# Optimization experiments

Hardware: AMD Instinct MI355X
Metric: run time of the kernel (lower is better)

## Reference

```python
import jax, jax.numpy as jnp
import numpy as np

N_NODES = 50000
N_EDGES = 1_600_000
IN_DIM, OUT_DIM, N_HEADS = 256, 64, 4
EPS = 1e-12  # F.normalize eps


def setup_inputs() -> dict:
    key = jax.random.key(0)
    k1, k2, k3, k4, k5 = jax.random.split(key, 5)
    h = jax.random.normal(k1, (N_NODES, IN_DIM), dtype=jnp.float32)
    edge_index = jax.random.randint(k2, (2, N_EDGES), 0, N_NODES, dtype=jnp.int32)
    # small scale keeps exp(leaky_relu(.)) well-conditioned (mimics xavier init)
    W = jax.random.normal(k3, (IN_DIM, OUT_DIM), dtype=jnp.float32) * 0.05
    Wl = jax.random.normal(k4, (N_HEADS, OUT_DIM), dtype=jnp.float32) * 0.05
    Wr = jax.random.normal(k5, (N_HEADS, OUT_DIM), dtype=jnp.float32) * 0.05
    b = jnp.zeros((OUT_DIM,), dtype=jnp.float32)
    return {"h": h, "W": W, "Wl": Wl, "Wr": Wr, "b": b, "edge_index": edge_index}


def reference(h, W, Wl, Wr, b, edge_index):
    N = h.shape[0]
    H = Wl.shape[0]
    x = h @ W                      # [N, D]
    el = x @ Wl.T                  # [N, H]
    er = x @ Wr.T                  # [N, H]
    src, dst = edge_index[0], edge_index[1]
    e = el[src] + er[dst]          # [E, H]
    e = jnp.exp(jax.nn.leaky_relu(e, negative_slope=0.2))
    # L1 row normalization over edges == F.normalize(dense_scatter, p=1, dim=-1)
    rowsum = jax.ops.segment_sum(e, src, num_segments=N)          # [N, H]
    w = e / jnp.maximum(rowsum, EPS)[src]                          # [E, H]
    # SpMM aggregation, per head to bound peak memory
    heads = [jax.ops.segment_sum(w[:, hd:hd + 1] * x[dst], src, num_segments=N)
             for hd in range(H)]
    out = jnp.stack(heads, axis=1)                                 # [N, H, D]
    out = jax.nn.elu(out + b)
    return out.reshape(N, H * x.shape[1])                          # [N, H*D]
```

## Files before the change

kernel.cpp:

```cpp
#include <hip/hip_runtime.h>
#include <hip/hip_bf16.h>
#include <hip/hip_fp16.h>

#define N_NODES 50000
#define N_EDGES 1600000
#define NPB    50
#define NBUK   1000
#define NSL    8
#define BCAPS  320
#define BCAPH  1280
#define GEMMB  782
#define PARTB  512
#define CHUNK  3125
#define BD     8

typedef __attribute__((ext_vector_type(8))) short short8;
typedef __attribute__((ext_vector_type(4))) float f32x4;

__device__ __forceinline__ unsigned short f2bf(float f) {
  union { float f; unsigned int i; } v; v.f = f;
  unsigned int i = v.i;
  unsigned int r = i + 0x7FFFu + ((i >> 16) & 1u);
  return (unsigned short)(r >> 16);
}

__global__ __launch_bounds__(256) void k_xpart(const float* __restrict__ hmat,
    const float* __restrict__ Wmat,
    const float* __restrict__ Wl, const float* __restrict__ Wr,
    float* __restrict__ el, float* __restrict__ er,
    __half* __restrict__ x16,
    const int* __restrict__ ei, int* __restrict__ bcnt,
    unsigned int* __restrict__ raw) {
  __shared__ __align__(16) char smem[36864];
  const int t = threadIdx.x;
  if (blockIdx.x >= PARTB) {
    unsigned short* Wt = (unsigned short*)smem;
    for (int idx = t; idx < 64 * 256; idx += 256) {
      int k = idx >> 6, n = idx & 63;
      Wt[n * 264 + k] = f2bf(Wmat[idx]);
    }
    __syncthreads();
    const int wave = t >> 6, lane = t & 63;
    const int quad = lane >> 4, l16 = lane & 15;
    const int m0 = (blockIdx.x - PARTB) * 64 + wave * 16;
    int arow = m0 + l16; if (arow >= N_NODES) arow = N_NODES - 1;
    f32x4 c[4] = {{0,0,0,0},{0,0,0,0},{0,0,0,0},{0,0,0,0}};
    const float* aptr = hmat + (size_t)arow * 256 + quad * 8;
    #pragma unroll
    for (int kb = 0; kb < 8; ++kb) {
      f32x4 a0 = *(const f32x4*)(aptr + kb * 32);
      f32x4 a1 = *(const f32x4*)(aptr + kb * 32 + 4);
      short8 a;
      a[0] = (short)f2bf(a0[0]); a[1] = (short)f2bf(a0[1]);
      a[2] = (short)f2bf(a0[2]); a[3] = (short)f2bf(a0[3]);
      a[4] = (short)f2bf(a1[0]); a[5] = (short)f2bf(a1[1]);
      a[6] = (short)f2bf(a1[2]); a[7] = (short)f2bf(a1[3]);
      #pragma unroll
      for (int nt = 0; nt < 4; ++nt) {
        int n = nt * 16 + l16;
        short8 b = *(const short8*)(&Wt[n * 264 + kb * 32 + quad * 8]);
        c[nt] = __builtin_amdgcn_mfma_f32_16x16x32_bf16(a, b, c[nt], 0, 0, 0);
      }
    }
    float wlv[4][4], wrv[4][4];
    #pragma unroll
    for (int h = 0; h < 4; ++h)
      #pragma unroll
      for (int nt = 0; nt < 4; ++nt) {
        wlv[h][nt] = Wl[h * 64 + nt * 16 + l16];
        wrv[h][nt] = Wr[h * 64 + nt * 16 + l16];
      }
    #pragma unroll
    for (int r = 0; r < 4; ++r) {
      const int grow = m0 + quad * 4 + r;
      const bool ok = grow < N_NODES;
      #pragma unroll
      for (int nt = 0; nt < 4; ++nt)
        if (ok) x16[grow * 64 + nt * 16 + l16] = __float2half(c[nt][r]);
      #pragma unroll
      for (int h = 0; h < 4; ++h) {
        float pl = c[0][r] * wlv[h][0];
        pl = fmaf(c[1][r], wlv[h][1], pl);
        pl = fmaf(c[2][r], wlv[h][2], pl);
        pl = fmaf(c[3][r], wlv[h][3], pl);
        float pr = c[0][r] * wrv[h][0];
        pr = fmaf(c[1][r], wrv[h][1], pr);
        pr = fmaf(c[2][r], wrv[h][2], pr);
        pr = fmaf(c[3][r], wrv[h][3], pr);
        #pragma unroll
        for (int off = 1; off < 16; off <<= 1) {
          pl += __shfl_xor(pl, off, 64);
          pr += __shfl_xor(pr, off, 64);
        }
        if (ok && l16 == 0) { el[grow * 4 + h] = pl; er[grow * 4 + h] = pr; }
      }
    }
  } else {
    int* scnt = (int*)smem;
    unsigned int* sbin = (unsigned int*)(smem + 4000);
    const int pj = blockIdx.x;
    const int slice = blockIdx.x & 7;
    for (int i = t; i < NBUK; i += 256) scnt[i] = 0;
    __syncthreads();
    const int e0 = pj * CHUNK;
    for (int e = e0 + t; e < e0 + CHUNK; e += 256) {
      int s = ei[e], d = ei[N_EDGES + e];
      int b = s / NPB;
      int sl = s - b * NPB;
      unsigned int val = ((unsigned int)d << 8) | (unsigned int)sl;
      int p = atomicAdd(&scnt[b], 1);
      if (p < BD) {
        sbin[b * BD + p] = val;
      } else {
        int cell = b * NSL + slice;
        int gp = atomicAdd(&bcnt[cell * 16], 1);
        if (gp < BCAPS) raw[(size_t)cell * BCAPS + gp] = val;
      }
    }
    __syncthreads();
    for (int b = t; b < NBUK; b += 256) {
      int c = scnt[b]; if (c > BD) c = BD;
      if (c > 0) {
        int cell = b * NSL + slice;
        int gp = atomicAdd(&bcnt[cell * 16], c);
        for (int k = 0; k < c; ++k) {
          int idx = gp + k;
          if (idx < BCAPS) raw[(size_t)cell * BCAPS + idx] = sbin[b * BD + k];
        }
      }
    }
  }
}

__global__ __launch_bounds__(256) void k_bucket(const unsigned int* __restrict__ raw,
    const int* __restrict__ bcnt,
    const float* __restrict__ el, const float* __restrict__ er,
    int* __restrict__ dlist, uint2* __restrict__ wts,
    int* __restrict__ rs_s, int* __restrict__ rs_e) {
  __shared__ unsigned int sraw[BCAPH];
  __shared__ int pref[NPB + 1];
  __shared__ int cur[NPB];
  const int b = blockIdx.x >> 1, H = blockIdx.x & 1, t = threadIdx.x;
  const int s0 = H * 4;
  int c0 = bcnt[(b * NSL + s0 + 0) * 16]; if (c0 > BCAPS) c0 = BCAPS;
  int c1 = bcnt[(b * NSL + s0 + 1) * 16]; if (c1 > BCAPS) c1 = BCAPS;
  int c2 = bcnt[(b * NSL + s0 + 2) * 16]; if (c2 > BCAPS) c2 = BCAPS;
  int c3 = bcnt[(b * NSL + s0 + 3) * 16]; if (c3 > BCAPS) c3 = BCAPS;
  const int o1 = c0, o2 = c0 + c1, o3 = c0 + c1 + c2, cnt = o3 + c3;
  if (t <= NPB) pref[t] = 0;
  __syncthreads();
  for (int j = t; j < c0; j += 256) { unsigned int r = raw[(size_t)(b*NSL+s0+0)*BCAPS + j]; sraw[j]      = r; atomicAdd(&pref[(int)(r & 255u) + 1], 1); }
  for (int j = t; j < c1; j += 256) { unsigned int r = raw[(size_t)(b*NSL+s0+1)*BCAPS + j]; sraw[o1 + j] = r; atomicAdd(&pref[(int)(r & 255u) + 1], 1); }
  for (int j = t; j < c2; j += 256) { unsigned int r = raw[(size_t)(b*NSL+s0+2)*BCAPS + j]; sraw[o2 + j] = r; atomicAdd(&pref[(int)(r & 255u) + 1], 1); }
  for (int j = t; j < c3; j += 256) { unsigned int r = raw[(size_t)(b*NSL+s0+3)*BCAPS + j]; sraw[o3 + j] = r; atomicAdd(&pref[(int)(r & 255u) + 1], 1); }
  __syncthreads();
  if (t == 0) {
    int run = 0;
    #pragma unroll
    for (int n = 0; n <= NPB; ++n) { run += pref[n]; pref[n] = run; }
  }
  __syncthreads();
  const int wbase = (b * 2 + H) * BCAPH;
  if (t < NPB) {
    cur[t] = pref[t];
    rs_s[H * N_NODES + b * NPB + t] = wbase + pref[t];
    rs_e[H * N_NODES + b * NPB + t] = wbase + pref[t + 1];
  }
  __syncthreads();
  const int base = b * NPB;
  for (int j = t; j < cnt; j += 256) {
    unsigned int r = sraw[j];
    int sl = (int)(r & 255u);
    int d  = (int)(r >> 8);
    int pos = atomicAdd(&cur[sl], 1);
    f32x4 a = ((const f32x4*)el)[base + sl];
    f32x4 e = ((const f32x4*)er)[d];
    float w[4];
    #pragma unroll
    for (int hh = 0; hh < 4; ++hh) {
      float tt = a[hh] + e[hh];
      tt = (tt >= 0.f) ? tt : 0.2f * tt;
      w[hh] = __expf(tt);
    }
    union { __half2 h; unsigned int i; } u01, u23;
    u01.h = __floats2half2_rn(w[0], w[1]);
    u23.h = __floats2half2_rn(w[2], w[3]);
    dlist[wbase + pos] = d;
    wts[wbase + pos] = make_uint2(u01.i, u23.i);
  }
}

__global__ __launch_bounds__(256) void k_agg(const __half* __restrict__ x16,
    const int* __restrict__ rs_s, const int* __restrict__ rs_e,
    const int* __restrict__ dlist, const uint2* __restrict__ wts,
    const float* __restrict__ bvec, float* __restrict__ out) {
  const int node = (blockIdx.x * 256 + threadIdx.x) >> 6;
  const int lane = threadIdx.x & 63;
  if (node >= N_NODES) return;
  float n0 = 0.f, n1 = 0.f, n2 = 0.f, n3 = 0.f;
  float d0 = 0.f, d1 = 0.f, d2 = 0.f, d3 = 0.f;
  #pragma unroll
  for (int hf = 0; hf < 2; ++hf) {
    const int j0 = __builtin_amdgcn_readfirstlane(rs_s[hf * N_NODES + node]);
    const int j1 = __builtin_amdgcn_readfirstlane(rs_e[hf * N_NODES + node]);
    #pragma unroll 4
    for (int j = j0; j < j1; ++j) {
      const int dd = dlist[j];
      const uint2 hw = wts[j];
      union { unsigned int i; __half2 h; } u01, u23;
      u01.i = hw.x; u23.i = hw.y;
      float2 f01 = __half22float2(u01.h);
      float2 f23 = __half22float2(u23.h);
      const __half* rowp = x16 + ((size_t)dd << 6);
      float xv = __half2float(rowp[lane]);
      d0 += f01.x; d1 += f01.y; d2 += f23.x; d3 += f23.y;
      n0 = fmaf(f01.x, xv, n0); n1 = fmaf(f01.y, xv, n1);
      n2 = fmaf(f23.x, xv, n2); n3 = fmaf(f23.y, xv, n3);
    }
  }
  float bv = bvec[lane];
  size_t ob = (size_t)node * 256 + lane;
  float o;
  o = n0 / fmaxf(d0, 1e-12f) + bv; o = (o > 0.f) ? o : (__expf(o) - 1.f); out[ob      ] = o;
  o = n1 / fmaxf(d1, 1e-12f) + bv; o = (o > 0.f) ? o : (__expf(o) - 1.f); out[ob +  64] = o;
  o = n2 / fmaxf(d2, 1e-12f) + bv; o = (o > 0.f) ? o : (__expf(o) - 1.f); out[ob + 128] = o;
  o = n3 / fmaxf(d3, 1e-12f) + bv; o = (o > 0.f) ? o : (__expf(o) - 1.f); out[ob + 192] = o;
}

extern "C" void kernel_launch(void* const* d_in, const int* in_sizes, int n_in,
                              void* d_out, int out_size, void* d_ws, size_t ws_size,
                              hipStream_t stream) {
  const float* h  = (const float*)d_in[0];
  const float* W  = (const float*)d_in[1];
  const float* Wl = (const float*)d_in[2];
  const float* Wr = (const float*)d_in[3];
  const float* b  = (const float*)d_in[4];
  const int*   ei = (const int*)d_in[5];
  float* out = (float*)d_out;

  char* ws = (char*)d_ws;
  float*        el    = (float*)       (ws + 0);
  float*        er    = (float*)       (ws + 800000);
  int*          bcnt  = (int*)         (ws + 1600000);
  unsigned int* raw   = (unsigned int*)(ws + 2112000);
  int*          dlist = (int*)         (ws + 12352000);
  uint2*        wts   = (uint2*)       (ws + 22592000);
  int*          rs_s  = (int*)         (ws + 43072000);
  int*          rs_e  = (int*)         (ws + 43472000);
  __half*       x16   = (__half*)      (ws + 43872000);
  (void)ws_size; (void)in_sizes; (void)n_in; (void)out_size;

  hipMemsetAsync(bcnt, 0, 512000, stream);

  k_xpart  <<<PARTB + GEMMB, 256, 0, stream>>>(h, W, Wl, Wr, el, er, x16, ei, bcnt, raw);
  k_bucket <<<2000,  256, 0, stream>>>(raw, bcnt, el, er, dlist, wts, rs_s, rs_e);
  k_agg    <<<12500, 256, 0, stream>>>(x16, rs_s, rs_e, dlist, wts, b, out);
}
```

Baseline: 218.0 us.

## Fold W into attention projections and move x GEMM beside bucketing

Attention logits el/er are now computed straight from h using precomposed W·Wlᵀ and W·Wrᵀ vectors in fp32. That lets the first kernel run only the edge partition plus a cheap per-node dot product. The bf16 MFMA GEMM that produces x16 moves into the second kernel and runs alongside the bucketing blocks, rebalancing work across the two launches. It changes el/er precision (fp32 instead of the bf16 GEMM path) and makes h be read twice.

```diff
diff --git a/kernel.cpp b/kernel.cpp
--- a/kernel.cpp
+++ b/kernel.cpp
@@ -11,6 +11,8 @@
 #define BCAPH  1280
 #define GEMMB  782
 #define PARTB  512
+#define ELERB  391
+#define BUKB   2000
 #define CHUNK  3125
 #define BD     8
 
@@ -24,78 +26,15 @@
   return (unsigned short)(r >> 16);
 }
 
-__global__ __launch_bounds__(256) void k_xpart(const float* __restrict__ hmat,
+__global__ __launch_bounds__(256) void k_peler(const float* __restrict__ hmat,
     const float* __restrict__ Wmat,
     const float* __restrict__ Wl, const float* __restrict__ Wr,
-    float* __restrict__ el, float* __restrict__ er,
-    __half* __restrict__ x16,
     const int* __restrict__ ei, int* __restrict__ bcnt,
-    unsigned int* __restrict__ raw) {
+    unsigned int* __restrict__ raw,
+    float* __restrict__ el, float* __restrict__ er) {
   __shared__ __align__(16) char smem[36864];
   const int t = threadIdx.x;
-  if (blockIdx.x >= PARTB) {
-    unsigned short* Wt = (unsigned short*)smem;
-    for (int idx = t; idx < 64 * 256; idx += 256) {
-      int k = idx >> 6, n = idx & 63;
-      Wt[n * 264 + k] = f2bf(Wmat[idx]);
-    }
-    __syncthreads();
-    const int wave = t >> 6, lane = t & 63;
-    const int quad = lane >> 4, l16 = lane & 15;
-    const int m0 = (blockIdx.x - PARTB) * 64 + wave * 16;
-    int arow = m0 + l16; if (arow >= N_NODES) arow = N_NODES - 1;
-    f32x4 c[4] = {{0,0,0,0},{0,0,0,0},{0,0,0,0},{0,0,0,0}};
-    const float* aptr = hmat + (size_t)arow * 256 + quad * 8;
-    #pragma unroll
-    for (int kb = 0; kb < 8; ++kb) {
-      f32x4 a0 = *(const f32x4*)(aptr + kb * 32);
-      f32x4 a1 = *(const f32x4*)(aptr + kb * 32 + 4);
-      short8 a;
-      a[0] = (short)f2bf(a0[0]); a[1] = (short)f2bf(a0[1]);
-      a[2] = (short)f2bf(a0[2]); a[3] = (short)f2bf(a0[3]);
-      a[4] = (short)f2bf(a1[0]); a[5] = (short)f2bf(a1[1]);
-      a[6] = (short)f2bf(a1[2]); a[7] = (short)f2bf(a1[3]);
-      #pragma unroll
-      for (int nt = 0; nt < 4; ++nt) {
-        int n = nt * 16 + l16;
-        short8 b = *(const short8*)(&Wt[n * 264 + kb * 32 + quad * 8]);
-        c[nt] = __builtin_amdgcn_mfma_f32_16x16x32_bf16(a, b, c[nt], 0, 0, 0);
-      }
-    }
-    float wlv[4][4], wrv[4][4];
-    #pragma unroll
-    for (int h = 0; h < 4; ++h)
-      #pragma unroll
-      for (int nt = 0; nt < 4; ++nt) {
-        wlv[h][nt] = Wl[h * 64 + nt * 16 + l16];
-        wrv[h][nt] = Wr[h * 64 + nt * 16 + l16];
-      }
-    #pragma unroll
-    for (int r = 0; r < 4; ++r) {
-      const int grow = m0 + quad * 4 + r;
-      const bool ok = grow < N_NODES;
-      #pragma unroll
-      for (int nt = 0; nt < 4; ++nt)
-        if (ok) x16[grow * 64 + nt * 16 + l16] = __float2half(c[nt][r]);
-      #pragma unroll
-      for (int h = 0; h < 4; ++h) {
-        float pl = c[0][r] * wlv[h][0];
-        pl = fmaf(c[1][r], wlv[h][1], pl);
-        pl = fmaf(c[2][r], wlv[h][2], pl);
-        pl = fmaf(c[3][r], wlv[h][3], pl);
-        float pr = c[0][r] * wrv[h][0];
-        pr = fmaf(c[1][r], wrv[h][1], pr);
-        pr = fmaf(c[2][r], wrv[h][2], pr);
-        pr = fmaf(c[3][r], wrv[h][3], pr);
-        #pragma unroll
-        for (int off = 1; off < 16; off <<= 1) {
-          pl += __shfl_xor(pl, off, 64);
-          pr += __shfl_xor(pr, off, 64);
-        }
-        if (ok && l16 == 0) { el[grow * 4 + h] = pl; er[grow * 4 + h] = pr; }
-      }
-    }
-  } else {
+  if (blockIdx.x < PARTB) {
     int* scnt = (int*)smem;
     unsigned int* sbin = (unsigned int*)(smem + 4000);
     const int pj = blockIdx.x;
@@ -129,64 +68,151 @@
         }
       }
     }
+  } else {
+    const int lane = t & 63;
+    float wfl[4][4] = {{0,0,0,0},{0,0,0,0},{0,0,0,0},{0,0,0,0}};
+    float wfr[4][4] = {{0,0,0,0},{0,0,0,0},{0,0,0,0},{0,0,0,0}};
+    for (int n = 0; n < 64; ++n) {
+      float wlv[4], wrv[4];
+      #pragma unroll
+      for (int h = 0; h < 4; ++h) { wlv[h] = Wl[h * 64 + n]; wrv[h] = Wr[h * 64 + n]; }
+      #pragma unroll
+      for (int c = 0; c < 4; ++c) {
+        float wv = Wmat[(lane * 4 + c) * 64 + n];
+        #pragma unroll
+        for (int h = 0; h < 4; ++h) {
+          wfl[c][h] = fmaf(wv, wlv[h], wfl[c][h]);
+          wfr[c][h] = fmaf(wv, wrv[h], wfr[c][h]);
+        }
+      }
+    }
+    const int gw = ((blockIdx.x - PARTB) * 256 + t) >> 6;
+    const int nw = ELERB * 4;
+    for (int node = gw; node < N_NODES; node += nw) {
+      f32x4 hv = *(const f32x4*)(hmat + (size_t)node * 256 + lane * 4);
+      float al[4] = {0, 0, 0, 0}, ar[4] = {0, 0, 0, 0};
+      #pragma unroll
+      for (int c = 0; c < 4; ++c)
+        #pragma unroll
+        for (int h = 0; h < 4; ++h) {
+          al[h] = fmaf(hv[c], wfl[c][h], al[h]);
+          ar[h] = fmaf(hv[c], wfr[c][h], ar[h]);
+        }
+      #pragma unroll
+      for (int off = 32; off > 0; off >>= 1)
+        #pragma unroll
+        for (int h = 0; h < 4; ++h) {
+          al[h] += __shfl_xor(al[h], off, 64);
+          ar[h] += __shfl_xor(ar[h], off, 64);
+        }
+      if (lane == 0) {
+        f32x4 pv = {al[0], al[1], al[2], al[3]};
+        f32x4 qv = {ar[0], ar[1], ar[2], ar[3]};
+        ((f32x4*)el)[node] = pv;
+        ((f32x4*)er)[node] = qv;
+      }
+    }
   }
 }
 
-__global__ __launch_bounds__(256) void k_bucket(const unsigned int* __restrict__ raw,
-    const int* __restrict__ bcnt,
+__global__ __launch_bounds__(256) void k_bgemm(const float* __restrict__ hmat,
+    const float* __restrict__ Wmat,
+    const unsigned int* __restrict__ raw, const int* __restrict__ bcnt,
     const float* __restrict__ el, const float* __restrict__ er,
+    __half* __restrict__ x16,
     int* __restrict__ dlist, uint2* __restrict__ wts,
     int* __restrict__ rs_s, int* __restrict__ rs_e) {
-  __shared__ unsigned int sraw[BCAPH];
-  __shared__ int pref[NPB + 1];
-  __shared__ int cur[NPB];
-  const int b = blockIdx.x >> 1, H = blockIdx.x & 1, t = threadIdx.x;
-  const int s0 = H * 4;
-  int c0 = bcnt[(b * NSL + s0 + 0) * 16]; if (c0 > BCAPS) c0 = BCAPS;
-  int c1 = bcnt[(b * NSL + s0 + 1) * 16]; if (c1 > BCAPS) c1 = BCAPS;
-  int c2 = bcnt[(b * NSL + s0 + 2) * 16]; if (c2 > BCAPS) c2 = BCAPS;
-  int c3 = bcnt[(b * NSL + s0 + 3) * 16]; if (c3 > BCAPS) c3 = BCAPS;
-  const int o1 = c0, o2 = c0 + c1, o3 = c0 + c1 + c2, cnt = o3 + c3;
-  if (t <= NPB) pref[t] = 0;
-  __syncthreads();
-  for (int j = t; j < c0; j += 256) { unsigned int r = raw[(size_t)(b*NSL+s0+0)*BCAPS + j]; sraw[j]      = r; atomicAdd(&pref[(int)(r & 255u) + 1], 1); }
-  for (int j = t; j < c1; j += 256) { unsigned int r = raw[(size_t)(b*NSL+s0+1)*BCAPS + j]; sraw[o1 + j] = r; atomicAdd(&pref[(int)(r & 255u) + 1], 1); }
-  for (int j = t; j < c2; j += 256) { unsigned int r = raw[(size_t)(b*NSL+s0+2)*BCAPS + j]; sraw[o2 + j] = r; atomicAdd(&pref[(int)(r & 255u) + 1], 1); }
-  for (int j = t; j < c3; j += 256) { unsigned int r = raw[(size_t)(b*NSL+s0+3)*BCAPS + j]; sraw[o3 + j] = r; atomicAdd(&pref[(int)(r & 255u) + 1], 1); }
-  __syncthreads();
-  if (t == 0) {
-    int run = 0;
+  __shared__ __align__(16) char smem[36864];
+  const int t = threadIdx.x;
+  if (blockIdx.x >= BUKB) {
+    unsigned short* Wt = (unsigned short*)smem;
+    for (int idx = t; idx < 64 * 256; idx += 256) {
+      int k = idx >> 6, n = idx & 63;
+      Wt[n * 264 + k] = f2bf(Wmat[idx]);
+    }
+    __syncthreads();
+    const int wave = t >> 6, lane = t & 63;
+    const int quad = lane >> 4, l16 = lane & 15;
+    const int m0 = (blockIdx.x - BUKB) * 64 + wave * 16;
+    int arow = m0 + l16; if (arow >= N_NODES) arow = N_NODES - 1;
+    f32x4 c[4] = {{0,0,0,0},{0,0,0,0},{0,0,0,0},{0,0,0,0}};
+    const float* aptr = hmat + (size_t)arow * 256 + quad * 8;
     #pragma unroll
-    for (int n = 0; n <= NPB; ++n) { run += pref[n]; pref[n] = run; }
-  }
-  __syncthreads();
-  const int wbase = (b * 2 + H) * BCAPH;
-  if (t < NPB) {
-    cur[t] = pref[t];
-    rs_s[H * N_NODES + b * NPB + t] = wbase + pref[t];
-    rs_e[H * N_NODES + b * NPB + t] = wbase + pref[t + 1];
-  }
-  __syncthreads();
-  const int base = b * NPB;
-  for (int j = t; j < cnt; j += 256) {
-    unsigned int r = sraw[j];
-    int sl = (int)(r & 255u);
-    int d  = (int)(r >> 8);
-    int pos = atomicAdd(&cur[sl], 1);
-    f32x4 a = ((const f32x4*)el)[base + sl];
-    f32x4 e = ((const f32x4*)er)[d];
-    float w[4];
+    for (int kb = 0; kb < 8; ++kb) {
+      f32x4 a0 = *(const f32x4*)(aptr + kb * 32);
+      f32x4 a1 = *(const f32x4*)(aptr + kb * 32 + 4);
+      short8 a;
+      a[0] = (short)f2bf(a0[0]); a[1] = (short)f2bf(a0[1]);
+      a[2] = (short)f2bf(a0[2]); a[3] = (short)f2bf(a0[3]);
+      a[4] = (short)f2bf(a1[0]); a[5] = (short)f2bf(a1[1]);
+      a[6] = (short)f2bf(a1[2]); a[7] = (short)f2bf(a1[3]);
+      #pragma unroll
+      for (int nt = 0; nt < 4; ++nt) {
+        int n = nt * 16 + l16;
+        short8 b = *(const short8*)(&Wt[n * 264 + kb * 32 + quad * 8]);
+        c[nt] = __builtin_amdgcn_mfma_f32_16x16x32_bf16(a, b, c[nt], 0, 0, 0);
+      }
+    }
     #pragma unroll
-    for (int hh = 0; hh < 4; ++hh) {
-      float tt = a[hh] + e[hh];
-      tt = (tt >= 0.f) ? tt : 0.2f * tt;
-      w[hh] = __expf(tt);
-    }
-    union { __half2 h; unsigned int i; } u01, u23;
-    u01.h = __floats2half2_rn(w[0], w[1]);
-    u23.h = __floats2half2_rn(w[2], w[3]);
-    dlist[wbase + pos] = d;
-    wts[wbase + pos] = make_uint2(u01.i, u23.i);
+    for (int nt = 0; nt < 4; ++nt) {
+      #pragma unroll
+      for (int r = 0; r < 4; ++r) {
+        int grow = m0 + quad * 4 + r;
+        if (grow < N_NODES) x16[grow * 64 + nt * 16 + l16] = __float2half(c[nt][r]);
+      }
+    }
+  } else {
+    unsigned int* sraw = (unsigned int*)smem;
+    int* pref = (int*)(smem + BCAPH * 4);
+    int* cur  = (int*)(smem + BCAPH * 4 + (NPB + 1) * 4);
+    const int b = blockIdx.x >> 1, H = blockIdx.x & 1;
+    const int s0 = H * 4;
+    int c0 = bcnt[(b * NSL + s0 + 0) * 16]; if (c0 > BCAPS) c0 = BCAPS;
+    int c1 = bcnt[(b * NSL + s0 + 1) * 16]; if (c1 > BCAPS) c1 = BCAPS;
+    int c2 = bcnt[(b * NSL + s0 + 2) * 16]; if (c2 > BCAPS) c2 = BCAPS;
+    int c3 = bcnt[(b * NSL + s0 + 3) * 16]; if (c3 > BCAPS) c3 = BCAPS;
+    const int o1 = c0, o2 = c0 + c1, o3 = c0 + c1 + c2, cnt = o3 + c3;
+    if (t <= NPB) pref[t] = 0;
+    __syncthreads();
+    for (int j = t; j < c0; j += 256) { unsigned int r = raw[(size_t)(b*NSL+s0+0)*BCAPS + j]; sraw[j]      = r; atomicAdd(&pref[(int)(r & 255u) + 1], 1); }
+    for (int j = t; j < c1; j += 256) { unsigned int r = raw[(size_t)(b*NSL+s0+1)*BCAPS + j]; sraw[o1 + j] = r; atomicAdd(&pref[(int)(r & 255u) + 1], 1); }
+    for (int j = t; j < c2; j += 256) { unsigned int r = raw[(size_t)(b*NSL+s0+2)*BCAPS + j]; sraw[o2 + j] = r; atomicAdd(&pref[(int)(r & 255u) + 1], 1); }
+    for (int j = t; j < c3; j += 256) { unsigned int r = raw[(size_t)(b*NSL+s0+3)*BCAPS + j]; sraw[o3 + j] = r; atomicAdd(&pref[(int)(r & 255u) + 1], 1); }
+    __syncthreads();
+    if (t == 0) {
+      int run = 0;
+      #pragma unroll
+      for (int n = 0; n <= NPB; ++n) { run += pref[n]; pref[n] = run; }
+    }
+    __syncthreads();
+    const int wbase = (b * 2 + H) * BCAPH;
+    if (t < NPB) {
+      cur[t] = pref[t];
+      rs_s[H * N_NODES + b * NPB + t] = wbase + pref[t];
+      rs_e[H * N_NODES + b * NPB + t] = wbase + pref[t + 1];
+    }
+    __syncthreads();
+    const int base = b * NPB;
+    for (int j = t; j < cnt; j += 256) {
+      unsigned int r = sraw[j];
+      int sl = (int)(r & 255u);
+      int d  = (int)(r >> 8);
+      int pos = atomicAdd(&cur[sl], 1);
+      f32x4 a = ((const f32x4*)el)[base + sl];
+      f32x4 e = ((const f32x4*)er)[d];
+      float w[4];
+      #pragma unroll
+      for (int hh = 0; hh < 4; ++hh) {
+        float tt = a[hh] + e[hh];
+        tt = (tt >= 0.f) ? tt : 0.2f * tt;
+        w[hh] = __expf(tt);
+      }
+      union { __half2 h; unsigned int i; } u01, u23;
+      u01.h = __floats2half2_rn(w[0], w[1]);
+      u23.h = __floats2half2_rn(w[2], w[3]);
+      dlist[wbase + pos] = d;
+      wts[wbase + pos] = make_uint2(u01.i, u23.i);
+    }
   }
 }
 
@@ -252,7 +278,7 @@
 
   hipMemsetAsync(bcnt, 0, 512000, stream);
 
-  k_xpart  <<<PARTB + GEMMB, 256, 0, stream>>>(h, W, Wl, Wr, el, er, x16, ei, bcnt, raw);
-  k_bucket <<<2000,  256, 0, stream>>>(raw, bcnt, el, er, dlist, wts, rs_s, rs_e);
-  k_agg    <<<12500, 256, 0, stream>>>(x16, rs_s, rs_e, dlist, wts, b, out);
-}
+  k_peler <<<PARTB + ELERB, 256, 0, stream>>>(h, W, Wl, Wr, ei, bcnt, raw, el, er);
+  k_bgemm <<<BUKB + GEMMB,  256, 0, stream>>>(h, W, raw, bcnt, el, er, x16, dlist, wts, rs_s, rs_e);
+  k_agg   <<<12500,         256, 0, stream>>>(x16, rs_s, rs_e, dlist, wts, b, out);
+}
```

Result: slower. 277.5 us (+27.3%).
